# Kernel optimization log

Hardware: AMD Instinct MI355X
Metric: run time of the kernel (lower is better)

The kernel has to match this reference:

```python
import jax, jax.numpy as jnp
import numpy as np

EPS = 1e-07


def setup_inputs() -> dict:
    key = jax.random.key(0)
    k1, k2, k3 = jax.random.split(key, 3)
    N, C, H, W = 2, 64, 540, 960
    tenIn = jax.random.normal(k1, (N, C, H, W), dtype=jnp.float32)
    tenFlow = jax.random.normal(k2, (N, 2, H, W), dtype=jnp.float32)
    tenMetric = jax.random.normal(k3, (N, 1, H, W), dtype=jnp.float32)
    return {"tenIn": tenIn, "tenFlow": tenFlow, "tenMetric": tenMetric}


def _splat(x, tenFlow):
    # x: [N, C, H, W] (C includes the appended normalization channel)
    N, C, H, W = x.shape
    gridY, gridX = jnp.meshgrid(jnp.arange(H, dtype=x.dtype),
                                jnp.arange(W, dtype=x.dtype), indexing='ij')
    fltX = gridX[None] + tenFlow[:, 0]  # [N, H, W]
    fltY = gridY[None] + tenFlow[:, 1]
    finite = jnp.isfinite(fltX) & jnp.isfinite(fltY)
    fltX = jnp.where(finite, fltX, 0.0)
    fltY = jnp.where(finite, fltY, 0.0)

    nwX = jnp.floor(fltX)
    nwY = jnp.floor(fltY)
    # bilinear corner weights (NW, NE, SW, SE)
    wNW = (nwX + 1.0 - fltX) * (nwY + 1.0 - fltY)
    wNE = (fltX - nwX) * (nwY + 1.0 - fltY)
    wSW = (nwX + 1.0 - fltX) * (fltY - nwY)
    wSE = (fltX - nwX) * (fltY - nwY)
    ix = nwX.astype(jnp.int32)
    iy = nwY.astype(jnp.int32)

    x_flat = x.transpose(0, 2, 3, 1).reshape(-1, C)  # [N*H*W, C]
    base = (jnp.arange(N, dtype=jnp.int32) * (H * W))[:, None, None]  # [N,1,1]
    out = jnp.zeros((N * H * W, C), dtype=x.dtype)
    for dx, dy, w in ((0, 0, wNW), (1, 0, wNE), (0, 1, wSW), (1, 1, wSE)):
        cx = ix + dx
        cy = iy + dy
        valid = finite & (cx >= 0) & (cx < W) & (cy >= 0) & (cy < H)
        ww = jnp.where(valid, w, 0.0).reshape(-1)  # masked weight: invalid -> 0
        idx = (base + jnp.clip(cy, 0, H - 1) * W + jnp.clip(cx, 0, W - 1)).reshape(-1)
        out = out.at[idx].add(x_flat * ww[:, None])
    return out.reshape(N, H, W, C).transpose(0, 3, 1, 2)


def reference(tenIn, tenFlow, tenMetric):
    # mode == 'soft': weight by exp(metric), append weight channel, splat, normalize
    m = jnp.exp(tenMetric)                      # [N,1,H,W]
    x = jnp.concatenate([tenIn * m, m], axis=1)  # [N,C+1,H,W]
    out = _splat(x, tenFlow)
    # mode_sub is None -> add-eps normalization
    return out[:, :-1] / (out[:, -1:] + EPS)
```

## Files before the change

### kernel.cpp

```cpp
#include <hip/hip_runtime.h>
#include <hip/hip_fp16.h>
#include <math.h>

constexpr int N_ = 2, C_ = 64, H_ = 540, W_ = 960;
constexpr int HW_ = H_ * W_;
constexpr int TSX = 32, TSY = 16;
constexpr int R_  = 8;
constexpr int WSX = TSX + 2 * R_;
constexpr int WSY = TSY + 2 * R_;
constexpr int WN  = WSX * WSY;
constexpr int K_  = 18;
constexpr int KP  = 19;
constexpr int NT  = 512;
constexpr int GX  = W_ / TSX;
constexpr int GY  = (H_ + TSY - 1) / TSY;
constexpr int NB  = N_ * GX * GY;
constexpr int APB = 256;
#define EPS_ 1e-7f

__global__ void __launch_bounds__(256, 4)
transpose_fp16(const float* __restrict__ in, __half* __restrict__ ws)
{
    __shared__ __half lh[APB][C_ + 4];
    const int t = threadIdx.x;
    const long pg0 = (long)blockIdx.x * APB;
    const int n  = (int)(pg0 / HW_);
    const int p0 = (int)(pg0 % HW_);

    const float* base = in + (size_t)n * C_ * HW_ + p0 + t;
    #pragma unroll
    for (int c = 0; c < C_; ++c)
        lh[t][c] = __float2half(base[(size_t)c * HW_]);
    __syncthreads();

    uint2* wsw = (uint2*)(ws + pg0 * C_);
    #pragma unroll
    for (int i = 0; i < 16; ++i) {
        int j   = i * 256 + t;
        int pix = j >> 4;
        int c0  = (j & 15) * 4;
        wsw[j] = *(const uint2*)&lh[pix][c0];
    }
}

__global__ void __launch_bounds__(NT, 6)
softsplat_gather(const __half* __restrict__ ws,
                 const float* __restrict__ flow,
                 const float* __restrict__ metric,
                 float* __restrict__ out)
{
    __shared__ unsigned hl[NT * KP];
    __shared__ unsigned cnt[NT];
    __shared__ float    txp[TSX][C_ + 1];

    const int bid = blockIdx.x;
    const int lin = (bid & 7) * (NB / 8) + (bid >> 3);
    const int by  = lin % GY;
    const int bx  = (lin / GY) % GX;
    const int n   = lin / (GY * GX);
    const int ty0 = by * TSY, tx0 = bx * TSX;
    const int t   = threadIdx.x;
    const int tileH = min(TSY, H_ - ty0);

    cnt[t] = 0;
    __syncthreads();

    const float* flowx = flow + (size_t)(n * 2 + 0) * HW_;
    const float* flowy = flow + (size_t)(n * 2 + 1) * HW_;
    const float* met   = metric + (size_t)n * HW_;

    #pragma unroll
    for (int it = 0; it < WN / NT; ++it) {
        int widx = t + it * NT;
        int wy = widx / WSX, wx = widx - wy * WSX;
        int sy = ty0 - R_ + wy;
        int sx = tx0 - R_ + wx;
        if (sx < 0 || sx >= W_ || sy < 0 || sy >= H_) continue;
        int sp = sy * W_ + sx;
        float fx = (float)sx + flowx[sp];
        float fy = (float)sy + flowy[sp];
        if (!(isfinite(fx) && isfinite(fy))) continue;
        float m = expf(met[sp]);

        float nwx = floorf(fx), nwy = floorf(fy);
        int   ix = (int)nwx, iy = (int)nwy;
        float ax = fx - nwx, ay = fy - nwy;
        float bw = 1.0f - ax, cw = 1.0f - ay;

        float w4[4]  = { bw * cw, ax * cw, bw * ay, ax * ay };
        int   cx4[4] = { ix, ix + 1, ix,     ix + 1 };
        int   cy4[4] = { iy, iy,     iy + 1, iy + 1 };

        #pragma unroll
        for (int k = 0; k < 4; ++k) {
            int cx = cx4[k], cy = cy4[k];
            if (cx < tx0 || cx >= tx0 + TSX || cy < ty0 || cy >= ty0 + tileH) continue;
            float we = w4[k] * m;
            if (we == 0.0f) continue;
            int d   = (cy - ty0) * TSX + (cx - tx0);
            int dsp = (sy - cy) * W_ + (sx - cx);
            unsigned slot = atomicAdd(&cnt[d], 1u);
            if (slot < (unsigned)K_)
                hl[d * KP + slot] = (__float_as_uint(we) & 0xFFFFC000u)
                                  | (unsigned)(dsp + 8192);
        }
    }
    __syncthreads();

    const int c_ = (int)min(cnt[t], (unsigned)K_);
    {
        float norm = 0.0f;
        for (int k = 0; k < c_; ++k)
            norm += __uint_as_float(hl[t * KP + k] & 0xFFFFC000u);
        const float inv = 1.0f / (norm + EPS_);
        for (int k = 0; k < c_; ++k) {
            unsigned b = hl[t * KP + k];
            float w = __uint_as_float(b & 0xFFFFC000u) * inv;
            hl[t * KP + k] = (__float_as_uint(w) & 0xFFFFC000u) | (b & 0x3FFFu);
        }
    }
    __syncthreads();

    const int l = t & 15, g = t >> 4;
    const int du = t & 31, cb = t >> 5;
    const __half* wsn = ws + (size_t)n * HW_ * C_;

    for (int pass = 0; pass < TSY; ++pass) {
        const int d   = pass * TSX + g;
        const int c_d = (int)min(cnt[d], (unsigned)K_);
        const unsigned* hld = &hl[d * KP];
        const int pdest = (ty0 + pass) * W_ + (tx0 + g);
        const __half* wsd = wsn + (size_t)pdest * C_ + l * 4;
        float acc0 = 0.f, acc1 = 0.f, acc2 = 0.f, acc3 = 0.f;
        for (int k0 = 0; k0 < c_d; k0 += 4) {
            uint2 raw[4];
            float wv[4];
            #pragma unroll
            for (int j = 0; j < 4; ++j) {
                unsigned b = (k0 + j < c_d) ? hld[k0 + j] : 0x00002000u;
                wv[j] = __uint_as_float(b & 0xFFFFC000u);
                int dsp = (int)(b & 0x3FFFu) - 8192;
                raw[j] = *(const uint2*)(wsd + (size_t)dsp * C_);
            }
            #pragma unroll
            for (int j = 0; j < 4; ++j) {
                const float2 f0 = __half22float2(*(const __half2*)&raw[j].x);
                const float2 f1 = __half22float2(*(const __half2*)&raw[j].y);
                acc0 += wv[j] * f0.x; acc1 += wv[j] * f0.y;
                acc2 += wv[j] * f1.x; acc3 += wv[j] * f1.y;
            }
        }
        txp[g][l * 4 + 0] = acc0;
        txp[g][l * 4 + 1] = acc1;
        txp[g][l * 4 + 2] = acc2;
        txp[g][l * 4 + 3] = acc3;
        __syncthreads();
        if (pass < tileH) {
            float* op = out + (size_t)n * C_ * HW_ + (size_t)(ty0 + pass) * W_ + tx0 + du;
            #pragma unroll
            for (int i = 0; i < 4; ++i) {
                int c = cb * 4 + i;
                op[(size_t)c * HW_] = txp[du][c];
            }
        }
        __syncthreads();
    }
}

__global__ void __launch_bounds__(NT, 8)
softsplat_direct(const float* __restrict__ in,
                 const float* __restrict__ flow,
                 const float* __restrict__ metric,
                 float* __restrict__ out)
{
    __shared__ unsigned hl[NT * KP];
    __shared__ unsigned cnt[NT];

    const int bid = blockIdx.x;
    const int lin = (bid & 7) * (NB / 8) + (bid >> 3);
    const int by  = lin % GY;
    const int bx  = (lin / GY) % GX;
    const int n   = lin / (GY * GX);
    const int ty0 = by * TSY, tx0 = bx * TSX;
    const int t   = threadIdx.x;
    const int tileH = min(TSY, H_ - ty0);

    cnt[t] = 0;
    __syncthreads();

    const float* flowx = flow + (size_t)(n * 2 + 0) * HW_;
    const float* flowy = flow + (size_t)(n * 2 + 1) * HW_;
    const float* met   = metric + (size_t)n * HW_;

    #pragma unroll
    for (int it = 0; it < WN / NT; ++it) {
        int widx = t + it * NT;
        int wy = widx / WSX, wx = widx - wy * WSX;
        int sy = ty0 - R_ + wy;
        int sx = tx0 - R_ + wx;
        if (sx < 0 || sx >= W_ || sy < 0 || sy >= H_) continue;
        int sp = sy * W_ + sx;
        float fx = (float)sx + flowx[sp];
        float fy = (float)sy + flowy[sp];
        if (!(isfinite(fx) && isfinite(fy))) continue;
        float m = expf(met[sp]);
        float nwx = floorf(fx), nwy = floorf(fy);
        int   ix = (int)nwx, iy = (int)nwy;
        float ax = fx - nwx, ay = fy - nwy;
        float bw = 1.0f - ax, cw = 1.0f - ay;
        float w4[4]  = { bw * cw, ax * cw, bw * ay, ax * ay };
        int   cx4[4] = { ix, ix + 1, ix,     ix + 1 };
        int   cy4[4] = { iy, iy,     iy + 1, iy + 1 };
        #pragma unroll
        for (int k = 0; k < 4; ++k) {
            int cx = cx4[k], cy = cy4[k];
            if (cx < tx0 || cx >= tx0 + TSX || cy < ty0 || cy >= ty0 + tileH) continue;
            float we = w4[k] * m;
            if (we == 0.0f) continue;
            int d   = (cy - ty0) * TSX + (cx - tx0);
            int dsp = (sy - cy) * W_ + (sx - cx);
            unsigned slot = atomicAdd(&cnt[d], 1u);
            if (slot < (unsigned)K_)
                hl[d * KP + slot] = (__float_as_uint(we) & 0xFFFFC000u)
                                  | (unsigned)(dsp + 8192);
        }
    }
    __syncthreads();

    const int c_ = (int)min(cnt[t], (unsigned)K_);
    float norm = 0.0f;
    for (int k = 0; k < c_; ++k)
        norm += __uint_as_float(hl[t * KP + k] & 0xFFFFC000u);
    const float inv = 1.0f / (norm + EPS_);
    for (int k = 0; k < c_; ++k) {
        unsigned b = hl[t * KP + k];
        float w = __uint_as_float(b & 0xFFFFC000u) * inv;
        hl[t * KP + k] = (__float_as_uint(w) & 0xFFFFC000u) | (b & 0x3FFFu);
    }
    int cmax = c_;
    #pragma unroll
    for (int o = 32; o; o >>= 1) cmax = max(cmax, __shfl_xor(cmax, o));

    const int dv = t >> 5, du = t & 31;
    const bool vOK = dv < tileH;
    const int v = min(ty0 + dv, H_ - 1);
    const int p = v * W_ + (tx0 + du);
    const float* inb  = in  + (size_t)n * C_ * HW_ + p;
    float*       outp = out + (size_t)n * C_ * HW_ + p;

    for (int q = 0; q < 16; ++q) {
        const float* bq = inb + (size_t)q * 4 * HW_;
        float acc[4] = {};
        #pragma unroll 2
        for (int k = 0; k < cmax; ++k) {
            if (k < c_) {
                unsigned b = hl[t * KP + k];
                float w   = __uint_as_float(b & 0xFFFFC000u);
                int   dsp = (int)(b & 0x3FFFu) - 8192;
                const float* s = bq + dsp;
                #pragma unroll
                for (int i = 0; i < 4; ++i) acc[i] += w * s[(size_t)i * HW_];
            }
        }
        if (vOK) {
            #pragma unroll
            for (int i = 0; i < 4; ++i)
                outp[(size_t)(q * 4 + i) * HW_] = acc[i];
        }
    }
}

extern "C" void kernel_launch(void* const* d_in, const int* in_sizes, int n_in,
                              void* d_out, int out_size, void* d_ws, size_t ws_size,
                              hipStream_t stream)
{
    const float* tenIn     = (const float*)d_in[0];
    const float* tenFlow   = (const float*)d_in[1];
    const float* tenMetric = (const float*)d_in[2];
    float* out = (float*)d_out;

    const size_t wsNeed = (size_t)N_ * HW_ * C_ * sizeof(__half);
    if (ws_size >= wsNeed) {
        __half* ws = (__half*)d_ws;
        transpose_fp16<<<N_ * HW_ / APB, 256, 0, stream>>>(tenIn, ws);
        softsplat_gather<<<NB, NT, 0, stream>>>(ws, tenFlow, tenMetric, out);
    } else {
        softsplat_direct<<<NB, NT, 0, stream>>>(tenIn, tenFlow, tenMetric, out);
    }
}
```

Before: 266.3 us.

## Replace block-wide transpose barriers with per-wave transpose and float4 stores

The output phase of the gather kernel now lets each wavefront handle its own 4-pixel by 64-channel chunk. Results go through a per-wave shared buffer using only wave barriers instead of two __syncthreads per row, and are stored as float4 along the pixel dimension. This removes the block-wide synchronisation stalls across the 16 row passes and widens the global stores. In exchange, each wave writes 16-byte segments per channel instead of 128-byte row segments, which may reduce store coalescing.

```diff
diff --git a/kernel.cpp b/kernel.cpp
--- a/kernel.cpp
+++ b/kernel.cpp
@@ -51,7 +51,7 @@
 {
     __shared__ unsigned hl[NT * KP];
     __shared__ unsigned cnt[NT];
-    __shared__ float    txp[TSX][C_ + 1];
+    __shared__ float    txw[8][256];
 
     const int bid = blockIdx.x;
     const int lin = (bid & 7) * (NB / 8) + (bid >> 3);
@@ -121,49 +121,52 @@
     }
     __syncthreads();
 
-    const int l = t & 15, g = t >> 4;
-    const int du = t & 31, cb = t >> 5;
+    const int wv = t >> 6;
+    const int ln = t & 63;
+    const int g  = ln >> 4, l = ln & 15;
     const __half* wsn = ws + (size_t)n * HW_ * C_;
-
-    for (int pass = 0; pass < TSY; ++pass) {
-        const int d   = pass * TSX + g;
-        const int c_d = (int)min(cnt[d], (unsigned)K_);
+    float* outn = out + (size_t)n * C_ * HW_;
+
+    for (int p = 0; p < 16; ++p) {
+        const int row  = 2 * wv + (p >> 3);
+        const int col0 = (p & 7) * 4;
+        const int pix0 = (ty0 + row) * W_ + (tx0 + col0);
+        const int d    = row * TSX + col0 + g;
+        const int c_d  = (int)min(cnt[d], (unsigned)K_);
         const unsigned* hld = &hl[d * KP];
-        const int pdest = (ty0 + pass) * W_ + (tx0 + g);
-        const __half* wsd = wsn + (size_t)pdest * C_ + l * 4;
+        const __half* wsd = wsn + (size_t)(pix0 + g) * C_ + l * 4;
+
         float acc0 = 0.f, acc1 = 0.f, acc2 = 0.f, acc3 = 0.f;
         for (int k0 = 0; k0 < c_d; k0 += 4) {
             uint2 raw[4];
-            float wv[4];
+            float wv4[4];
             #pragma unroll
             for (int j = 0; j < 4; ++j) {
                 unsigned b = (k0 + j < c_d) ? hld[k0 + j] : 0x00002000u;
-                wv[j] = __uint_as_float(b & 0xFFFFC000u);
-                int dsp = (int)(b & 0x3FFFu) - 8192;
-                raw[j] = *(const uint2*)(wsd + (size_t)dsp * C_);
+                wv4[j] = __uint_as_float(b & 0xFFFFC000u);
+                ptrdiff_t dsp = (ptrdiff_t)(int)(b & 0x3FFFu) - 8192;
+                raw[j] = *(const uint2*)(wsd + dsp * C_);
             }
             #pragma unroll
             for (int j = 0; j < 4; ++j) {
                 const float2 f0 = __half22float2(*(const __half2*)&raw[j].x);
                 const float2 f1 = __half22float2(*(const __half2*)&raw[j].y);
-                acc0 += wv[j] * f0.x; acc1 += wv[j] * f0.y;
-                acc2 += wv[j] * f1.x; acc3 += wv[j] * f1.y;
+                acc0 += wv4[j] * f0.x; acc1 += wv4[j] * f0.y;
+                acc2 += wv4[j] * f1.x; acc3 += wv4[j] * f1.y;
             }
         }
-        txp[g][l * 4 + 0] = acc0;
-        txp[g][l * 4 + 1] = acc1;
-        txp[g][l * 4 + 2] = acc2;
-        txp[g][l * 4 + 3] = acc3;
-        __syncthreads();
-        if (pass < tileH) {
-            float* op = out + (size_t)n * C_ * HW_ + (size_t)(ty0 + pass) * W_ + tx0 + du;
-            #pragma unroll
-            for (int i = 0; i < 4; ++i) {
-                int c = cb * 4 + i;
-                op[(size_t)c * HW_] = txp[du][c];
-            }
-        }
-        __syncthreads();
+
+        __builtin_amdgcn_wave_barrier();
+        txw[wv][(4 * l + 0) * 4 + g] = acc0;
+        txw[wv][(4 * l + 1) * 4 + g] = acc1;
+        txw[wv][(4 * l + 2) * 4 + g] = acc2;
+        txw[wv][(4 * l + 3) * 4 + g] = acc3;
+        __builtin_amdgcn_wave_barrier();
+        const float4 o = *(const float4*)&txw[wv][ln * 4];
+        __builtin_amdgcn_wave_barrier();
+
+        if (row < tileH)
+            *(float4*)(outn + (size_t)ln * HW_ + pix0) = o;
     }
 }
 
```

New measurement: 429.1 us. 61.1% more time.
